# Kernel optimization log

Hardware: AMD Instinct MI355X
Metric: run time of the kernel (lower is better)

Reference implementation:

```python
import jax, jax.numpy as jnp
import numpy as np

B, S, D = 2, 2048, 1024
H, HD = 16, 64  # num_heads, head_dim; H*HD == D


def setup_inputs() -> dict:
    key = jax.random.key(0)
    ks = jax.random.split(key, 10)
    scale = 1.0 / np.sqrt(D)
    inputs_q = jax.random.normal(ks[0], (B, S, D), dtype=jnp.float32)
    inputs_kv = inputs_q  # self-attention
    Wq = jax.random.normal(ks[1], (D, H, HD), dtype=jnp.float32) * scale
    Wk = jax.random.normal(ks[2], (D, H, HD), dtype=jnp.float32) * scale
    Wv = jax.random.normal(ks[3], (D, H, HD), dtype=jnp.float32) * scale
    Wo = jax.random.normal(ks[4], (H, HD, D), dtype=jnp.float32) * scale
    bq = jnp.zeros((H, HD), dtype=jnp.float32)
    bk = jnp.zeros((H, HD), dtype=jnp.float32)
    bv = jnp.zeros((H, HD), dtype=jnp.float32)
    bo = jnp.zeros((D,), dtype=jnp.float32)
    return {"inputs_q": inputs_q, "inputs_kv": inputs_kv,
            "Wq": Wq, "bq": bq, "Wk": Wk, "bk": bk,
            "Wv": Wv, "bv": bv, "Wo": Wo, "bo": bo}


def reference(inputs_q, inputs_kv, Wq, bq, Wk, bk, Wv, bv, Wo, bo):
    # QKV projections: [B,S,D] x [D,H,HD] -> [B,S,H,HD]
    q = jnp.einsum('bsd,dhe->bshe', inputs_q, Wq) + bq
    k = jnp.einsum('bsd,dhe->bshe', inputs_kv, Wk) + bk
    v = jnp.einsum('bsd,dhe->bshe', inputs_kv, Wv) + bv
    # scale query by sqrt(depth) as in dot_product_attention
    q = q / jnp.sqrt(jnp.asarray(HD, dtype=q.dtype))
    # attention scores: [B,H,Sq,Sk]
    scores = jnp.einsum('bqhd,bkhd->bhqk', q, k)
    weights = jax.nn.softmax(scores, axis=-1)
    # weighted values: [B,Sq,H,HD]
    ctx = jnp.einsum('bhqk,bkhd->bqhd', weights, v)
    # output projection over (head, head_dim) axes
    out = jnp.einsum('bqhd,hde->bqe', ctx, Wo) + bo
    return out
```

## Files before the change

### kernel.cpp

```cpp
#include <hip/hip_runtime.h>
#include <hip/hip_bf16.h>

typedef __bf16 bf16x8 __attribute__((ext_vector_type(8)));
typedef __bf16 bf16x4 __attribute__((ext_vector_type(4)));
typedef float f32x4 __attribute__((ext_vector_type(4)));

#define MFMA(a,b,c) __builtin_amdgcn_mfma_f32_16x16x32_bf16(a,b,c,0,0,0)

__device__ __forceinline__ unsigned short f2bf(float f) {
    union { float f; unsigned u; } x; x.f = f;
    unsigned r = x.u + 0x7fffu + ((x.u >> 16) & 1u);
    return (unsigned short)(r >> 16);
}

__device__ __forceinline__ bf16x8 ld8(const unsigned short* p) {
    return *reinterpret_cast<const bf16x8*>(p);
}

__device__ __forceinline__ float exp2_fast(float x) {
    float r; asm("v_exp_f32 %0, %1" : "=v"(r) : "v"(x)); return r;
}

__device__ __forceinline__ void stage16(const unsigned short* g, unsigned short* l) {
    __builtin_amdgcn_global_load_lds(
        (const __attribute__((address_space(1))) unsigned int*)(const void*)(g),
        (__attribute__((address_space(3))) unsigned int*)(void*)(l),
        16, 0, 0);
}

__global__ void k_cvt(const float* __restrict__ in, unsigned short* __restrict__ out, int n4) {
    int i = blockIdx.x * blockDim.x + threadIdx.x;
    int stride = gridDim.x * blockDim.x;
    for (; i < n4; i += stride) {
        float4 v = reinterpret_cast<const float4*>(in)[i];
        ushort4 o;
        o.x = f2bf(v.x); o.y = f2bf(v.y); o.z = f2bf(v.z); o.w = f2bf(v.w);
        reinterpret_cast<ushort4*>(out)[i] = o;
    }
}

__global__ void k_cvt_t(const float* __restrict__ in, unsigned short* __restrict__ out) {
    __shared__ unsigned short tile[64][66];
    int t = threadIdx.x;
    int bk = (blockIdx.x & 15) * 64, bn = (blockIdx.x >> 4) * 64;
    #pragma unroll
    for (int r = 0; r < 16; ++r) {
        int k = (t >> 6) * 16 + r;
        int n = t & 63;
        tile[n][k] = f2bf(in[(bk + k) * 1024 + bn + n]);
    }
    __syncthreads();
    #pragma unroll
    for (int r = 0; r < 16; ++r) {
        int n = (t >> 6) * 16 + r;
        int k = t & 63;
        out[(bn + n) * 1024 + bk + k] = tile[n][k];
    }
}

template<int EPI>
__global__ __launch_bounds__(256) void k_gemm_s(
    const unsigned short* __restrict__ A,
    const unsigned short* __restrict__ Bt,
    const float* __restrict__ b0, const float* __restrict__ b1,
    const float* __restrict__ b2,
    unsigned short* __restrict__ q_out, unsigned short* __restrict__ k_out,
    unsigned short* __restrict__ v_out, float* __restrict__ f_out,
    int M, int N, int K)
{
    __shared__ __align__(16) unsigned short A_lds[2][128][32];
    __shared__ __align__(16) unsigned short B_lds[2][128][32];

    const int lane = threadIdx.x & 63;
    const int wave = threadIdx.x >> 6;
    const int wr = wave >> 1, wc = wave & 1;
    const int nbm = M >> 7;
    const int nwg = nbm * (N >> 7);
    int blk = blockIdx.x;
    blk = (blk & 7) * (nwg >> 3) + (blk >> 3);
    const int bm = (blk % nbm) << 7;
    const int bn = (blk / nbm) << 7;
    const int g = lane >> 4, r16 = lane & 15;

    const int srow = lane >> 2;
    const int schunk = lane & 3;
    const unsigned short* Asrc = A  + (size_t)(bm + wave * 32 + srow) * K + schunk * 8;
    const unsigned short* Bsrc = Bt + (size_t)(bn + wave * 32 + srow) * K + schunk * 8;

    auto stage = [&](int buf, int k0) {
        #pragma unroll
        for (int j = 0; j < 2; ++j) {
            stage16(Asrc + (size_t)(j * 16) * K + k0, &A_lds[buf][wave * 32 + j * 16][0]);
            stage16(Bsrc + (size_t)(j * 16) * K + k0, &B_lds[buf][wave * 32 + j * 16][0]);
        }
    };

    f32x4 acc[4][4] = {};

    stage(0, 0);
    __syncthreads();

    const int nsteps = K >> 5;
    for (int t = 0; t < nsteps; ++t) {
        const int cur = t & 1;
        if (t + 1 < nsteps) stage(cur ^ 1, (t + 1) * 32);

        bf16x8 a[4], b[4];
        #pragma unroll
        for (int i = 0; i < 4; ++i)
            a[i] = ld8(&A_lds[cur][wr * 64 + i * 16 + r16][g * 8]);
        #pragma unroll
        for (int j = 0; j < 4; ++j)
            b[j] = ld8(&B_lds[cur][wc * 64 + j * 16 + r16][g * 8]);
        #pragma unroll
        for (int i = 0; i < 4; ++i)
            #pragma unroll
            for (int j = 0; j < 4; ++j)
                acc[i][j] = MFMA(a[i], b[j], acc[i][j]);
        __syncthreads();
    }

    const int seg = bn >> 10;
    const float* bias = (EPI == 1) ? b0 : (seg == 0 ? b0 : (seg == 1 ? b1 : b2));
    const float scale = (EPI == 0 && seg == 0) ? 0.18033688011112042f : 1.0f;

    #pragma unroll
    for (int i = 0; i < 4; ++i)
        #pragma unroll
        for (int j = 0; j < 4; ++j) {
            const int mbase = bm + wr * 64 + i * 16 + g * 4;
            const int n = bn + wc * 64 + j * 16 + r16;
            if constexpr (EPI == 1) {
                #pragma unroll
                for (int r = 0; r < 4; ++r)
                    f_out[(size_t)(mbase + r) * N + n] = acc[i][j][r] + b0[n];
            } else {
                const int nl = n & 1023;
                const int h = nl >> 6, e = nl & 63;
                const int b_ = mbase >> 11, s0 = mbase & 2047;
                float vv[4];
                #pragma unroll
                for (int r = 0; r < 4; ++r)
                    vv[r] = (acc[i][j][r] + bias[nl]) * scale;
                if (seg == 2) {
                    bf16x4 pk = { (__bf16)vv[0], (__bf16)vv[1], (__bf16)vv[2], (__bf16)vv[3] };
                    *reinterpret_cast<bf16x4*>(
                        &v_out[(((size_t)(b_ * 16 + h) * 64 + e) * 2048) + s0]) = pk;
                } else {
                    unsigned short* o = (seg == 0) ? q_out : k_out;
                    #pragma unroll
                    for (int r = 0; r < 4; ++r)
                        o[(((size_t)(b_ * 16 + h) * 2048 + (s0 + r)) * 64) + e] = f2bf(vv[r]);
                }
            }
        }
}

__global__ __launch_bounds__(256) void k_attn(
    const unsigned short* __restrict__ Q,
    const unsigned short* __restrict__ Kb,
    const unsigned short* __restrict__ Vt,
    unsigned short* __restrict__ ctx)
{
    __shared__ __align__(16) unsigned short K_lds[2][64][64];
    __shared__ __align__(16) unsigned short V_lds[2][64][64];

    const int lane = threadIdx.x & 63;
    const int wave = threadIdx.x >> 6;
    const int g = lane >> 4, r16 = lane & 15;

    const int blk = blockIdx.x;
    const int x = blk & 7, i = blk >> 3;
    const int bh = x * 4 + (i & 3);
    const int qb = i >> 2;
    const int b = bh >> 4, h = bh & 15;
    const int q0 = qb * 64 + wave * 16;

    const unsigned short* Qp    = Q  + ((size_t)bh * 2048 + q0) * 64;
    const unsigned short* Khead = Kb + (size_t)bh * 2048 * 64;
    const unsigned short* Vhead = Vt + (size_t)bh * 64 * 2048;

    bf16x8 aq[2];
    #pragma unroll
    for (int h2 = 0; h2 < 2; ++h2)
        aq[h2] = ld8(Qp + (size_t)r16 * 64 + h2 * 32 + g * 8);

    bf16x8 ones;
    #pragma unroll
    for (int j = 0; j < 8; ++j) ones[j] = (__bf16)1.0f;

    const int srow = lane >> 3;

    auto stage = [&](int buf, int kt) {
        #pragma unroll
        for (int j = 0; j < 2; ++j) {
            const int r0 = wave * 16 + j * 8;
            const int sc = (lane & 7) ^ (srow & 3) ^ (j << 2);
            stage16(Khead + (size_t)(kt + r0 + srow) * 64 + sc * 8,
                    &K_lds[buf][r0][0]);
            stage16(Vhead + (size_t)(r0 + srow) * 2048 + kt + sc * 8,
                    &V_lds[buf][r0][0]);
        }
    };

    f32x4 o[4] = {};
    f32x4 sum_acc = {};

    const int krow_base = (r16 >> 2) * 8 + (r16 & 3);
    const int pik = (r16 & 3) | (((r16 >> 2) & 1) << 2);
    const int piv = (r16 & 3) | (((r16 >> 3) & 1) << 2);

    stage(0, 0);
    __syncthreads();

    for (int it = 0; it < 32; ++it) {
        const int cur = it & 1;
        if (it + 1 < 32) stage(cur ^ 1, (it + 1) * 64);

        f32x4 s[4] = {};
        #pragma unroll
        for (int c = 0; c < 4; ++c) {
            const int krow = 32 * (c >> 1) + (c & 1) * 4 + krow_base;
            bf16x8 bk0 = ld8(&K_lds[cur][krow][((g)     ^ pik) * 8]);
            bf16x8 bk1 = ld8(&K_lds[cur][krow][((4 + g) ^ pik) * 8]);
            s[c] = MFMA(bk0, aq[0], s[c]);
            s[c] = MFMA(bk1, aq[1], s[c]);
        }
        bf16x8 bv[4][2];
        #pragma unroll
        for (int n = 0; n < 4; ++n)
            #pragma unroll
            for (int ks = 0; ks < 2; ++ks)
                bv[n][ks] = ld8(&V_lds[cur][n * 16 + r16][((ks * 4 + g) ^ piv) * 8]);

        bf16x8 ap0, ap1;
        #pragma unroll
        for (int r = 0; r < 4; ++r) {
            ap0[r]     = (__bf16)exp2_fast(s[0][r]);
            ap0[4 + r] = (__bf16)exp2_fast(s[1][r]);
            ap1[r]     = (__bf16)exp2_fast(s[2][r]);
            ap1[4 + r] = (__bf16)exp2_fast(s[3][r]);
        }
        #pragma unroll
        for (int n = 0; n < 4; ++n) {
            o[n] = MFMA(ap0, bv[n][0], o[n]);
            o[n] = MFMA(ap1, bv[n][1], o[n]);
        }
        sum_acc = MFMA(ap0, ones, sum_acc);
        sum_acc = MFMA(ap1, ones, sum_acc);
        __syncthreads();
    }

    float inv[4];
    #pragma unroll
    for (int r = 0; r < 4; ++r) inv[r] = 1.0f / sum_acc[r];
    #pragma unroll
    for (int n = 0; n < 4; ++n)
        #pragma unroll
        for (int r = 0; r < 4; ++r) {
            int q = q0 + g * 4 + r;
            float v = o[n][r] * inv[r];
            ctx[((size_t)(b * 2048 + q)) * 1024 + h * 64 + n * 16 + r16] = f2bf(v);
        }
}

extern "C" void kernel_launch(void* const* d_in, const int* in_sizes, int n_in,
                              void* d_out, int out_size, void* d_ws, size_t ws_size,
                              hipStream_t stream)
{
    const float* xq  = (const float*)d_in[0];
    const float* Wq  = (const float*)d_in[2];
    const float* bq  = (const float*)d_in[3];
    const float* Wk  = (const float*)d_in[4];
    const float* bk  = (const float*)d_in[5];
    const float* Wv  = (const float*)d_in[6];
    const float* bv  = (const float*)d_in[7];
    const float* Wo  = (const float*)d_in[8];
    const float* bo  = (const float*)d_in[9];
    float* out = (float*)d_out;

    char* ws = (char*)d_ws;
    const size_t MB = 1024 * 1024;
    unsigned short* Xq_b   = (unsigned short*)(ws + 0);
    unsigned short* Wqkvt  = (unsigned short*)(ws + 16 * MB);
    unsigned short* Wot    = (unsigned short*)(ws + 22 * MB);
    unsigned short* Qb     = (unsigned short*)(ws + 24 * MB);
    unsigned short* Kbuf   = (unsigned short*)(ws + 32 * MB);
    unsigned short* Vt     = (unsigned short*)(ws + 40 * MB);
    unsigned short* Ctx    = (unsigned short*)(ws + 48 * MB);

    k_cvt<<<1024, 256, 0, stream>>>(xq, Xq_b, (4096 * 1024) / 4);
    k_cvt_t<<<256, 256, 0, stream>>>(Wq, Wqkvt);
    k_cvt_t<<<256, 256, 0, stream>>>(Wk, Wqkvt + 1024 * 1024);
    k_cvt_t<<<256, 256, 0, stream>>>(Wv, Wqkvt + 2 * 1024 * 1024);
    k_cvt_t<<<256, 256, 0, stream>>>(Wo, Wot);

    k_gemm_s<0><<<768, 256, 0, stream>>>(Xq_b, Wqkvt, bq, bk, bv,
                                         Qb, Kbuf, Vt, nullptr, 4096, 3072, 1024);

    k_attn<<<1024, 256, 0, stream>>>(Qb, Kbuf, Vt, Ctx);

    k_gemm_s<1><<<256, 256, 0, stream>>>(Ctx, Wot, bo, bo, bo,
                                         nullptr, nullptr, nullptr, out, 4096, 1024, 1024);
}
```

Before: 127.1 us.

## Load V fragments directly from global memory and pack bf16 via cvt_pk

Stops staging V tiles through LDS. Each lane now loads its V MFMA operand fragments straight from global memory (transposed V rows) at the top of the iteration, before the K prefetch is issued, so the loads overlap the QK MFMAs. Also replaces the per-element float-to-bf16 casts of the softmax probabilities with packed v_cvt_pk_bf16_f32 instructions. This cuts LDS traffic and footprint, but adds global/L2 load latency that sits in the critical path of each iteration, and each wave re-reads V that the block previously shared through LDS.

```diff
diff --git a/kernel.cpp b/kernel.cpp
--- a/kernel.cpp
+++ b/kernel.cpp
@@ -19,6 +19,12 @@
 
 __device__ __forceinline__ float exp2_fast(float x) {
     float r; asm("v_exp_f32 %0, %1" : "=v"(r) : "v"(x)); return r;
+}
+
+__device__ __forceinline__ unsigned cvt_pk_bf16(float lo, float hi) {
+    unsigned r;
+    asm("v_cvt_pk_bf16_f32 %0, %1, %2" : "=v"(r) : "v"(lo), "v"(hi));
+    return r;
 }
 
 __device__ __forceinline__ void stage16(const unsigned short* g, unsigned short* l) {
@@ -163,7 +169,6 @@
     unsigned short* __restrict__ ctx)
 {
     __shared__ __align__(16) unsigned short K_lds[2][64][64];
-    __shared__ __align__(16) unsigned short V_lds[2][64][64];
 
     const int lane = threadIdx.x & 63;
     const int wave = threadIdx.x >> 6;
@@ -179,6 +184,7 @@
     const unsigned short* Qp    = Q  + ((size_t)bh * 2048 + q0) * 64;
     const unsigned short* Khead = Kb + (size_t)bh * 2048 * 64;
     const unsigned short* Vhead = Vt + (size_t)bh * 64 * 2048;
+    const unsigned short* Vrow  = Vhead + (size_t)r16 * 2048 + g * 8;
 
     bf16x8 aq[2];
     #pragma unroll
@@ -198,8 +204,6 @@
             const int sc = (lane & 7) ^ (srow & 3) ^ (j << 2);
             stage16(Khead + (size_t)(kt + r0 + srow) * 64 + sc * 8,
                     &K_lds[buf][r0][0]);
-            stage16(Vhead + (size_t)(r0 + srow) * 2048 + kt + sc * 8,
-                    &V_lds[buf][r0][0]);
         }
     };
 
@@ -208,14 +212,22 @@
 
     const int krow_base = (r16 >> 2) * 8 + (r16 & 3);
     const int pik = (r16 & 3) | (((r16 >> 2) & 1) << 2);
-    const int piv = (r16 & 3) | (((r16 >> 3) & 1) << 2);
 
     stage(0, 0);
     __syncthreads();
 
     for (int it = 0; it < 32; ++it) {
         const int cur = it & 1;
-        if (it + 1 < 32) stage(cur ^ 1, (it + 1) * 64);
+        const int kt = it * 64;
+
+        bf16x8 bv[4][2];
+        #pragma unroll
+        for (int n = 0; n < 4; ++n)
+            #pragma unroll
+            for (int ks = 0; ks < 2; ++ks)
+                bv[n][ks] = ld8(Vrow + (size_t)(n * 16) * 2048 + kt + ks * 32);
+
+        if (it + 1 < 32) stage(cur ^ 1, kt + 64);
 
         f32x4 s[4] = {};
         #pragma unroll
@@ -226,28 +238,31 @@
             s[c] = MFMA(bk0, aq[0], s[c]);
             s[c] = MFMA(bk1, aq[1], s[c]);
         }
-        bf16x8 bv[4][2];
-        #pragma unroll
-        for (int n = 0; n < 4; ++n)
+
+        float p[4][4];
+        #pragma unroll
+        for (int c = 0; c < 4; ++c)
             #pragma unroll
-            for (int ks = 0; ks < 2; ++ks)
-                bv[n][ks] = ld8(&V_lds[cur][n * 16 + r16][((ks * 4 + g) ^ piv) * 8]);
-
-        bf16x8 ap0, ap1;
-        #pragma unroll
-        for (int r = 0; r < 4; ++r) {
-            ap0[r]     = (__bf16)exp2_fast(s[0][r]);
-            ap0[4 + r] = (__bf16)exp2_fast(s[1][r]);
-            ap1[r]     = (__bf16)exp2_fast(s[2][r]);
-            ap1[4 + r] = (__bf16)exp2_fast(s[3][r]);
-        }
+            for (int r = 0; r < 4; ++r)
+                p[c][r] = exp2_fast(s[c][r]);
+
+        union { bf16x8 v; unsigned u[4]; } A0, A1;
+        A0.u[0] = cvt_pk_bf16(p[0][0], p[0][1]);
+        A0.u[1] = cvt_pk_bf16(p[0][2], p[0][3]);
+        A0.u[2] = cvt_pk_bf16(p[1][0], p[1][1]);
+        A0.u[3] = cvt_pk_bf16(p[1][2], p[1][3]);
+        A1.u[0] = cvt_pk_bf16(p[2][0], p[2][1]);
+        A1.u[1] = cvt_pk_bf16(p[2][2], p[2][3]);
+        A1.u[2] = cvt_pk_bf16(p[3][0], p[3][1]);
+        A1.u[3] = cvt_pk_bf16(p[3][2], p[3][3]);
+
         #pragma unroll
         for (int n = 0; n < 4; ++n) {
-            o[n] = MFMA(ap0, bv[n][0], o[n]);
-            o[n] = MFMA(ap1, bv[n][1], o[n]);
-        }
-        sum_acc = MFMA(ap0, ones, sum_acc);
-        sum_acc = MFMA(ap1, ones, sum_acc);
+            o[n] = MFMA(A0.v, bv[n][0], o[n]);
+            o[n] = MFMA(A1.v, bv[n][1], o[n]);
+        }
+        sum_acc = MFMA(A0.v, ones, sum_acc);
+        sum_acc = MFMA(A1.v, ones, sum_acc);
         __syncthreads();
     }
 
```

New measurement: 202.2 us. 59.2% more time.
